# Kernel optimization log

Hardware: AMD Instinct MI355X
Metric: run time of the kernel (lower is better)

## Reference

```python
import jax, jax.numpy as jnp
import numpy as np

B, L, D = 8, 512, 128
SCALE = float(np.sqrt(D))


def setup_inputs() -> dict:
    key = jax.random.key(0)
    ks = jax.random.split(key, 12)
    s = 1.0 / np.sqrt(D)
    inp = {
        "query": jax.random.normal(ks[0], (B, L, D), jnp.float32),
        "key": jax.random.normal(ks[1], (B, L, D), jnp.float32),
        "value": jax.random.normal(ks[2], (B, L, D), jnp.float32),
        # nn.Linear weights stored torch-style as (out, in); y = x @ W.T + b
        "Wq": jax.random.uniform(ks[3], (D, D), jnp.float32, -s, s),
        "bq": jax.random.uniform(ks[4], (D,), jnp.float32, -s, s),
        "Wk": jax.random.uniform(ks[5], (D, D), jnp.float32, -s, s),
        "bk": jax.random.uniform(ks[6], (D,), jnp.float32, -s, s),
        "Wv": jax.random.uniform(ks[7], (D, D), jnp.float32, -s, s),
        "bv": jax.random.uniform(ks[8], (D,), jnp.float32, -s, s),
        "w_delta": jax.random.uniform(ks[9], (D,), jnp.float32, -s, s),
        "b_delta": jnp.zeros((), jnp.float32),
        "w_sigma": jax.random.uniform(ks[10], (D,), jnp.float32, -s, s),
        "b_sigma": jnp.zeros((), jnp.float32),
        "w_theta": jax.random.uniform(ks[11], (D,), jnp.float32, -s, s),
        "b_theta": jnp.zeros((), jnp.float32),
    }
    return inp


def reference(query, key, value, Wq, bq, Wk, bk, Wv, bv,
              w_delta, b_delta, w_sigma, b_sigma, w_theta, b_theta):
    Q = query @ Wq.T + bq          # [B,Lq,D]
    K = key @ Wk.T + bk            # [B,Lk,D]
    V = value @ Wv.T + bv          # [B,Lk,D]
    e = jnp.tanh(Q[:, :, None, :] + K[:, None, :, :])  # [B,Lq,Lk,D]
    # base (sum/scale) + three linear score heads fuse into one reduction over D
    w_all = 1.0 / SCALE + w_delta + w_sigma + w_theta   # [D]
    b_all = b_delta + b_sigma + b_theta
    combined = jnp.einsum('bqkd,d->bqk', e, w_all) + b_all
    attn = jax.nn.softmax(combined, axis=-1)            # dropout in eval mode: identity
    out = jnp.einsum('bqk,bkd->bqd', attn, V)
    return out
```

## Files before the change

### kernel.cpp

```cpp
#include <hip/hip_runtime.h>


#define BB 8
#define LL 512
#define DD 128
#define NROW (BB*LL)
#define MATN (NROW*DD)
#define KSPLIT 8

static constexpr float C1 = 2.8853900817779268f;
static constexpr float LOG2E = 1.4426950408889634f;
static constexpr float INV_SCALE = 0.08838834764831845f;

typedef float v2f __attribute__((ext_vector_type(2)));

__device__ __forceinline__ float fast_exp2(float x) { return __builtin_amdgcn_exp2f(x); }
__device__ __forceinline__ float fast_rcp(float x)  { return __builtin_amdgcn_rcpf(x); }

__device__ __forceinline__ v2f mk2(float a, float b) { v2f r; r.x = a; r.y = b; return r; }

__device__ __forceinline__ v2f fma2(v2f a, v2f b, v2f c) {
#if __has_builtin(__builtin_elementwise_fma)
    return __builtin_elementwise_fma(a, b, c);
#else
    v2f r; r.x = fmaf(a.x, b.x, c.x); r.y = fmaf(a.y, b.y, c.y); return r;
#endif
}

__global__ __launch_bounds__(256) void proj_kernel(
    const float* __restrict__ query, const float* __restrict__ key,
    const float* __restrict__ value,
    const float* __restrict__ Wq, const float* __restrict__ bq,
    const float* __restrict__ Wk, const float* __restrict__ bk,
    const float* __restrict__ Wv, const float* __restrict__ bv,
    const float* __restrict__ wd, const float* __restrict__ wsg,
    const float* __restrict__ wtt, float* __restrict__ ws)
{
    __shared__ __align__(16) float Wl[128 * 66];
    __shared__ __align__(16) float Xl[32 * 66];

    const int bx = blockIdx.x;
    const int m  = bx >> 7;
    const int r0 = (bx & 127) * 32;
    const float* X    = (m == 0) ? query : (m == 1) ? key : value;
    const float* W    = (m == 0) ? Wq    : (m == 1) ? Wk  : Wv;
    const float* bias = (m == 0) ? bq    : (m == 1) ? bk  : bv;
    const int t = threadIdx.x;

    if (bx == 0 && t < 128) {
        ws[(size_t)3 * MATN + t] =
            -2.0f * LOG2E * (INV_SCALE + wd[t] + wsg[t] + wtt[t]);
    }

    const int cg = t & 31;
    const int rg = t >> 5;

    v2f acc[4][4];
    #pragma unroll
    for (int j = 0; j < 4; ++j) {
        float bj = bias[cg + 32 * j];
        #pragma unroll
        for (int i = 0; i < 4; ++i) acc[i][j] = mk2(bj, 0.f);
    }

    const float4* Wsrc = (const float4*)W;
    const float4* Xsrc = (const float4*)X;

    for (int h = 0; h < 2; ++h) {
        __syncthreads();
        #pragma unroll
        for (int j = 0; j < 8; ++j) {
            int g = t + j * 256;
            int c = g >> 4, f4 = g & 15;
            float4 v = Wsrc[c * 32 + h * 16 + f4];
            float* dst = &Wl[c * 66 + f4 * 4];
            *(float2*)dst       = make_float2(v.x, v.y);
            *(float2*)(dst + 2) = make_float2(v.z, v.w);
        }
        #pragma unroll
        for (int j = 0; j < 2; ++j) {
            int g = t + j * 256;
            int r = g >> 4, f4 = g & 15;
            float4 v = Xsrc[(r0 + r) * 32 + h * 16 + f4];
            float* dst = &Xl[r * 66 + f4 * 4];
            *(float2*)dst       = make_float2(v.x, v.y);
            *(float2*)(dst + 2) = make_float2(v.z, v.w);
        }
        __syncthreads();

        #pragma unroll 4
        for (int dg = 0; dg < 32; ++dg) {
            v2f bf[4];
            #pragma unroll
            for (int j = 0; j < 4; ++j)
                bf[j] = *(const v2f*)&Wl[(cg + 32 * j) * 66 + 2 * dg];
            v2f af[4];
            #pragma unroll
            for (int i = 0; i < 4; ++i)
                af[i] = *(const v2f*)&Xl[(rg * 4 + i) * 66 + 2 * dg];
            #pragma unroll
            for (int i = 0; i < 4; ++i)
                #pragma unroll
                for (int j = 0; j < 4; ++j)
                    acc[i][j] = fma2(af[i], bf[j], acc[i][j]);
        }
    }

    if (m == 2) {
        float* oV = ws + (size_t)2 * MATN;
        #pragma unroll
        for (int i = 0; i < 4; ++i) {
            int r = r0 + rg * 4 + i;
            #pragma unroll
            for (int j = 0; j < 4; ++j)
                oV[(size_t)r * DD + cg + 32 * j] = acc[i][j].x + acc[i][j].y;
        }
    } else {
        float* oE = ws + (size_t)m * MATN;
        #pragma unroll
        for (int i = 0; i < 4; ++i) {
            int r = r0 + rg * 4 + i;
            #pragma unroll
            for (int j = 0; j < 4; ++j)
                oE[(size_t)r * DD + cg + 32 * j] =
                    fast_exp2(C1 * (acc[i][j].x + acc[i][j].y));
        }
    }
}

template <bool ATOMIC>
__global__ __launch_bounds__(512, 6) void attn_kernel(
    const float* __restrict__ ws, float* __restrict__ outp,
    float* __restrict__ psump)
{
    __shared__ __align__(16) float Ekt[64 * 132];
    __shared__ __align__(16) float wl[128];
    __shared__ __align__(16) float EqL[8 * 512];

    const float* Eq  = ws;
    const float* Ek  = ws + (size_t)MATN;
    const float* Vp  = ws + (size_t)2 * MATN;

    const int bx   = blockIdx.x;
    const int qblk = bx >> 3;
    const int kx   = bx & 7;
    const int b    = qblk >> 4;
    const int wave = __builtin_amdgcn_readfirstlane((int)threadIdx.x >> 6);
    const int lane = threadIdx.x & 63;
    const int qa   = qblk * 32 + wave * 4;
    const int eqo  = wave * 512;

    {
        const float4* EqW = (const float4*)(Eq + (size_t)qa * DD);
        float4 ea = EqW[2 * lane];
        float4 eb = EqW[2 * lane + 1];
        *(float4*)&EqL[eqo + 8 * lane]     = ea;
        *(float4*)&EqL[eqo + 8 * lane + 4] = eb;
    }

    {
        const float4* sK = (const float4*)(Ek + (size_t)b * (LL * DD)
                                              + (size_t)kx * 64 * DD);
        #pragma unroll
        for (int r = 0; r < 4; ++r) {
            int g = (int)threadIdx.x + r * 512;
            int row = g >> 5, c4 = g & 31;
            *(float4*)&Ekt[row * 132 + c4 * 4] = sK[g];
        }
        if (threadIdx.x < 32)
            ((float4*)wl)[threadIdx.x] =
                ((const float4*)(ws + (size_t)3 * MATN))[threadIdx.x];
    }
    __syncthreads();

    const float* krow = &Ekt[lane * 132];
    const float4* wl4 = (const float4*)wl;
    const float* eqp  = &EqL[eqo];
    float s0 = 0.f, s1 = 0.f, s2 = 0.f, s3 = 0.f;

    #pragma unroll 2
    for (int ih = 0; ih < 16; ++ih) {
        float4 k0 = *(const float4*)(krow + 8 * ih);
        float4 k1 = *(const float4*)(krow + 8 * ih + 4);
        float4 w0 = wl4[2 * ih];
        float4 w1 = wl4[2 * ih + 1];
        #define QT(SS, QQ) { \
            float4 A0 = *(const float4*)(eqp + QQ * 128 + 8 * ih); \
            float4 A1 = *(const float4*)(eqp + QQ * 128 + 8 * ih + 4); \
            float e0 = fmaf(A0.x, k0.x, 1.f), e1 = fmaf(A0.y, k0.y, 1.f); \
            float e2 = fmaf(A0.z, k0.z, 1.f), e3 = fmaf(A0.w, k0.w, 1.f); \
            float d01 = e0 * e1, d23 = e2 * e3; \
            float n01 = fmaf(w0.x, e1, w0.y * e0); \
            float n23 = fmaf(w0.z, e3, w0.w * e2); \
            float num = fmaf(n01, d23, n23 * d01); \
            SS = fmaf(num, fast_rcp(d01 * d23), SS); \
            float f0 = fmaf(A1.x, k1.x, 1.f), f1 = fmaf(A1.y, k1.y, 1.f); \
            float f2 = fmaf(A1.z, k1.z, 1.f), f3 = fmaf(A1.w, k1.w, 1.f); \
            float g01 = f0 * f1, g23 = f2 * f3; \
            float m01 = fmaf(w1.x, f1, w1.y * f0); \
            float m23 = fmaf(w1.z, f3, w1.w * f2); \
            float mum = fmaf(m01, g23, m23 * g01); \
            SS = fmaf(mum, fast_rcp(g01 * g23), SS); }
        QT(s0, 0) QT(s1, 1) QT(s2, 2) QT(s3, 3)
        #undef QT
    }
    float p0 = fast_exp2(s0);
    float p1 = fast_exp2(s1);
    float p2 = fast_exp2(s2);
    float p3 = fast_exp2(s3);

    float t0 = p0, t1 = p1, t2 = p2, t3 = p3;
    #pragma unroll
    for (int off = 32; off; off >>= 1) {
        t0 += __shfl_xor(t0, off);
        t1 += __shfl_xor(t1, off);
        t2 += __shfl_xor(t2, off);
        t3 += __shfl_xor(t3, off);
    }
    if (lane == 0) {
        if (ATOMIC) {
            atomicAdd(&psump[qa + 0], t0);
            atomicAdd(&psump[qa + 1], t1);
            atomicAdd(&psump[qa + 2], t2);
            atomicAdd(&psump[qa + 3], t3);
        } else {
            float* pp = psump + (size_t)kx * NROW + qa;
            pp[0] = t0; pp[1] = t1; pp[2] = t2; pp[3] = t3;
        }
    }

    *(float4*)&EqL[eqo + 4 * lane] = make_float4(p0, p1, p2, p3);

    const float2* __restrict__ Vg =
        (const float2*)(Vp + (size_t)b * (LL * DD) + (size_t)kx * 64 * DD);
    float2 o[4];
    #pragma unroll
    for (int qq = 0; qq < 4; ++qq) o[qq] = make_float2(0.f, 0.f);

    #pragma unroll
    for (int g = 0; g < 8; ++g) {
        float2 v[8];
        #pragma unroll
        for (int e = 0; e < 8; ++e)
            v[e] = Vg[(size_t)(8 * g + e) * 64 + lane];
        #pragma unroll
        for (int e = 0; e < 8; ++e) {
            int kidx = 8 * g + e;
            float4 pw = *(const float4*)&EqL[eqo + 4 * kidx];
            o[0].x = fmaf(pw.x, v[e].x, o[0].x); o[0].y = fmaf(pw.x, v[e].y, o[0].y);
            o[1].x = fmaf(pw.y, v[e].x, o[1].x); o[1].y = fmaf(pw.y, v[e].y, o[1].y);
            o[2].x = fmaf(pw.z, v[e].x, o[2].x); o[2].y = fmaf(pw.z, v[e].y, o[2].y);
            o[3].x = fmaf(pw.w, v[e].x, o[3].x); o[3].y = fmaf(pw.w, v[e].y, o[3].y);
        }
    }

    const int d2 = 2 * lane;
    if (ATOMIC) {
        #pragma unroll
        for (int qq = 0; qq < 4; ++qq) {
            atomicAdd(&outp[(size_t)(qa + qq) * DD + d2],     o[qq].x);
            atomicAdd(&outp[(size_t)(qa + qq) * DD + d2 + 1], o[qq].y);
        }
    } else {
        float* base = outp + (size_t)kx * MATN;
        #pragma unroll
        for (int qq = 0; qq < 4; ++qq)
            *(float2*)&base[(size_t)(qa + qq) * DD + d2] = o[qq];
    }
}

__global__ __launch_bounds__(256) void reduce_kernel(
    const float* __restrict__ part, const float* __restrict__ psumP,
    float* __restrict__ out)
{
    int t = blockIdx.x * 256 + threadIdx.x;
    const float4* p4 = (const float4*)part;
    float4 acc = make_float4(0.f, 0.f, 0.f, 0.f);
    #pragma unroll
    for (int kx = 0; kx < KSPLIT; ++kx) {
        float4 v = p4[(size_t)kx * (MATN / 4) + t];
        acc.x += v.x; acc.y += v.y; acc.z += v.z; acc.w += v.w;
    }
    int q = t >> 5;
    float s = 0.f;
    #pragma unroll
    for (int kx = 0; kx < KSPLIT; ++kx) s += psumP[(size_t)kx * NROW + q];
    float inv = fast_rcp(s);
    ((float4*)out)[t] = make_float4(acc.x * inv, acc.y * inv,
                                    acc.z * inv, acc.w * inv);
}

__global__ __launch_bounds__(256) void norm_kernel(
    float* __restrict__ out, const float* __restrict__ psumG)
{
    int t = blockIdx.x * 256 + threadIdx.x;
    float2* o2 = (float2*)out;
    int q = t >> 6;
    float inv = fast_rcp(psumG[q]);
    float2 v = o2[t];
    o2[t] = make_float2(v.x * inv, v.y * inv);
}

extern "C" void kernel_launch(void* const* d_in, const int* in_sizes, int n_in,
                              void* d_out, int out_size, void* d_ws, size_t ws_size,
                              hipStream_t stream) {
    const float* query = (const float*)d_in[0];
    const float* key_  = (const float*)d_in[1];
    const float* value = (const float*)d_in[2];
    const float* Wq    = (const float*)d_in[3];
    const float* bq    = (const float*)d_in[4];
    const float* Wk    = (const float*)d_in[5];
    const float* bk    = (const float*)d_in[6];
    const float* Wv    = (const float*)d_in[7];
    const float* bv    = (const float*)d_in[8];
    const float* wd    = (const float*)d_in[9];
    const float* wsg   = (const float*)d_in[11];
    const float* wtt   = (const float*)d_in[13];
    float* ws = (float*)d_ws;
    float* out = (float*)d_out;

    const size_t off_psum = (size_t)3 * MATN + 128;
    const size_t off_part = off_psum + (size_t)KSPLIT * NROW;
    const size_t need = (off_part + (size_t)KSPLIT * MATN) * sizeof(float);

    proj_kernel<<<384, 256, 0, stream>>>(query, key_, value,
                                         Wq, bq, Wk, bk, Wv, bv,
                                         wd, wsg, wtt, ws);
    if (ws_size >= need) {
        float* psumP = ws + off_psum;
        float* part  = ws + off_part;
        attn_kernel<false><<<1024, 512, 0, stream>>>(ws, part, psumP);
        reduce_kernel<<<512, 256, 0, stream>>>(part, psumP, out);
    } else {
        float* psumG = ws + off_psum;
        hipMemsetAsync(out, 0, (size_t)out_size * sizeof(float), stream);
        hipMemsetAsync(psumG, 0, (size_t)NROW * sizeof(float), stream);
        attn_kernel<true><<<1024, 512, 0, stream>>>(ws, out, psumG);
        norm_kernel<<<1024, 256, 0, stream>>>(out, psumG);
    }
}
```

Before: 135.2 us.

## Pack attention score math into v2f ops, drop Eq LDS staging, shrink proj tiles

The attention score loop is rewritten to use packed two-wide float FMAs, with the d-dimension permuted in Eq, Ek and the weight vector so pairs line up for the packed ops. The Eq LDS buffer is removed: query exponentials are read directly from global memory (wave-uniform) and the probabilities reuse the Ekt buffer after a barrier. This frees LDS to raise the occupancy hint from 6 to 8 blocks. The projection kernel halves its row tile to launch twice as many blocks, trading reuse of the weight tile for more parallelism.

```diff
diff --git a/kernel.cpp b/kernel.cpp
--- a/kernel.cpp
+++ b/kernel.cpp
@@ -25,6 +25,11 @@
 #else
     v2f r; r.x = fmaf(a.x, b.x, c.x); r.y = fmaf(a.y, b.y, c.y); return r;
 #endif
+}
+
+__device__ __forceinline__ int dperm(int c) {
+    const int pmap[4] = {0, 2, 1, 3};
+    return (c & ~3) | pmap[c & 3];
 }
 
 __global__ __launch_bounds__(256) void proj_kernel(
@@ -37,30 +42,30 @@
     const float* __restrict__ wtt, float* __restrict__ ws)
 {
     __shared__ __align__(16) float Wl[128 * 66];
-    __shared__ __align__(16) float Xl[32 * 66];
+    __shared__ __align__(16) float Xl[16 * 66];
 
     const int bx = blockIdx.x;
-    const int m  = bx >> 7;
-    const int r0 = (bx & 127) * 32;
+    const int m  = bx >> 8;
+    const int r0 = (bx & 255) * 16;
     const float* X    = (m == 0) ? query : (m == 1) ? key : value;
     const float* W    = (m == 0) ? Wq    : (m == 1) ? Wk  : Wv;
     const float* bias = (m == 0) ? bq    : (m == 1) ? bk  : bv;
     const int t = threadIdx.x;
 
     if (bx == 0 && t < 128) {
-        ws[(size_t)3 * MATN + t] =
+        ws[(size_t)3 * MATN + dperm(t)] =
             -2.0f * LOG2E * (INV_SCALE + wd[t] + wsg[t] + wtt[t]);
     }
 
     const int cg = t & 31;
     const int rg = t >> 5;
 
-    v2f acc[4][4];
+    v2f acc[2][4];
     #pragma unroll
     for (int j = 0; j < 4; ++j) {
         float bj = bias[cg + 32 * j];
         #pragma unroll
-        for (int i = 0; i < 4; ++i) acc[i][j] = mk2(bj, 0.f);
+        for (int i = 0; i < 2; ++i) acc[i][j] = mk2(bj, 0.f);
     }
 
     const float4* Wsrc = (const float4*)W;
@@ -77,10 +82,8 @@
             *(float2*)dst       = make_float2(v.x, v.y);
             *(float2*)(dst + 2) = make_float2(v.z, v.w);
         }
-        #pragma unroll
-        for (int j = 0; j < 2; ++j) {
-            int g = t + j * 256;
-            int r = g >> 4, f4 = g & 15;
+        {
+            int r = t >> 4, f4 = t & 15;
             float4 v = Xsrc[(r0 + r) * 32 + h * 16 + f4];
             float* dst = &Xl[r * 66 + f4 * 4];
             *(float2*)dst       = make_float2(v.x, v.y);
@@ -94,12 +97,12 @@
             #pragma unroll
             for (int j = 0; j < 4; ++j)
                 bf[j] = *(const v2f*)&Wl[(cg + 32 * j) * 66 + 2 * dg];
-            v2f af[4];
-            #pragma unroll
-            for (int i = 0; i < 4; ++i)
-                af[i] = *(const v2f*)&Xl[(rg * 4 + i) * 66 + 2 * dg];
-            #pragma unroll
-            for (int i = 0; i < 4; ++i)
+            v2f af[2];
+            #pragma unroll
+            for (int i = 0; i < 2; ++i)
+                af[i] = *(const v2f*)&Xl[(rg * 2 + i) * 66 + 2 * dg];
+            #pragma unroll
+            for (int i = 0; i < 2; ++i)
                 #pragma unroll
                 for (int j = 0; j < 4; ++j)
                     acc[i][j] = fma2(af[i], bf[j], acc[i][j]);
@@ -109,33 +112,33 @@
     if (m == 2) {
         float* oV = ws + (size_t)2 * MATN;
         #pragma unroll
-        for (int i = 0; i < 4; ++i) {
-            int r = r0 + rg * 4 + i;
+        for (int i = 0; i < 2; ++i) {
+            int r = r0 + rg * 2 + i;
             #pragma unroll
             for (int j = 0; j < 4; ++j)
                 oV[(size_t)r * DD + cg + 32 * j] = acc[i][j].x + acc[i][j].y;
         }
     } else {
         float* oE = ws + (size_t)m * MATN;
-        #pragma unroll
-        for (int i = 0; i < 4; ++i) {
-            int r = r0 + rg * 4 + i;
+        const int cp = dperm(cg);
+        #pragma unroll
+        for (int i = 0; i < 2; ++i) {
+            int r = r0 + rg * 2 + i;
             #pragma unroll
             for (int j = 0; j < 4; ++j)
-                oE[(size_t)r * DD + cg + 32 * j] =
+                oE[(size_t)r * DD + cp + 32 * j] =
                     fast_exp2(C1 * (acc[i][j].x + acc[i][j].y));
         }
     }
 }
 
 template <bool ATOMIC>
-__global__ __launch_bounds__(512, 6) void attn_kernel(
+__global__ __launch_bounds__(512, 8) void attn_kernel(
     const float* __restrict__ ws, float* __restrict__ outp,
     float* __restrict__ psump)
 {
     __shared__ __align__(16) float Ekt[64 * 132];
     __shared__ __align__(16) float wl[128];
-    __shared__ __align__(16) float EqL[8 * 512];
 
     const float* Eq  = ws;
     const float* Ek  = ws + (size_t)MATN;
@@ -148,15 +151,6 @@
     const int wave = __builtin_amdgcn_readfirstlane((int)threadIdx.x >> 6);
     const int lane = threadIdx.x & 63;
     const int qa   = qblk * 32 + wave * 4;
-    const int eqo  = wave * 512;
-
-    {
-        const float4* EqW = (const float4*)(Eq + (size_t)qa * DD);
-        float4 ea = EqW[2 * lane];
-        float4 eb = EqW[2 * lane + 1];
-        *(float4*)&EqL[eqo + 8 * lane]     = ea;
-        *(float4*)&EqL[eqo + 8 * lane + 4] = eb;
-    }
 
     {
         const float4* sK = (const float4*)(Ek + (size_t)b * (LL * DD)
@@ -175,39 +169,43 @@
 
     const float* krow = &Ekt[lane * 132];
     const float4* wl4 = (const float4*)wl;
-    const float* eqp  = &EqL[eqo];
-    float s0 = 0.f, s1 = 0.f, s2 = 0.f, s3 = 0.f;
+    const float* eqq  = Eq + (size_t)qa * DD;
+    v2f S0 = mk2(0.f, 0.f), S1 = S0, S2 = S0, S3 = S0;
 
     #pragma unroll 2
     for (int ih = 0; ih < 16; ++ih) {
-        float4 k0 = *(const float4*)(krow + 8 * ih);
-        float4 k1 = *(const float4*)(krow + 8 * ih + 4);
-        float4 w0 = wl4[2 * ih];
-        float4 w1 = wl4[2 * ih + 1];
+        float4 K0 = *(const float4*)(krow + 8 * ih);
+        float4 K1 = *(const float4*)(krow + 8 * ih + 4);
+        float4 W0 = wl4[2 * ih];
+        float4 W1 = wl4[2 * ih + 1];
+        v2f k0lo = mk2(K0.x, K0.y), k0hi = mk2(K0.z, K0.w);
+        v2f k1lo = mk2(K1.x, K1.y), k1hi = mk2(K1.z, K1.w);
+        v2f w0lo = mk2(W0.x, W0.y), w0hi = mk2(W0.z, W0.w);
+        v2f w1lo = mk2(W1.x, W1.y), w1hi = mk2(W1.z, W1.w);
         #define QT(SS, QQ) { \
-            float4 A0 = *(const float4*)(eqp + QQ * 128 + 8 * ih); \
-            float4 A1 = *(const float4*)(eqp + QQ * 128 + 8 * ih + 4); \
-            float e0 = fmaf(A0.x, k0.x, 1.f), e1 = fmaf(A0.y, k0.y, 1.f); \
-            float e2 = fmaf(A0.z, k0.z, 1.f), e3 = fmaf(A0.w, k0.w, 1.f); \
-            float d01 = e0 * e1, d23 = e2 * e3; \
-            float n01 = fmaf(w0.x, e1, w0.y * e0); \
-            float n23 = fmaf(w0.z, e3, w0.w * e2); \
-            float num = fmaf(n01, d23, n23 * d01); \
-            SS = fmaf(num, fast_rcp(d01 * d23), SS); \
-            float f0 = fmaf(A1.x, k1.x, 1.f), f1 = fmaf(A1.y, k1.y, 1.f); \
-            float f2 = fmaf(A1.z, k1.z, 1.f), f3 = fmaf(A1.w, k1.w, 1.f); \
-            float g01 = f0 * f1, g23 = f2 * f3; \
-            float m01 = fmaf(w1.x, f1, w1.y * f0); \
-            float m23 = fmaf(w1.z, f3, w1.w * f2); \
-            float mum = fmaf(m01, g23, m23 * g01); \
-            SS = fmaf(mum, fast_rcp(g01 * g23), SS); }
-        QT(s0, 0) QT(s1, 1) QT(s2, 2) QT(s3, 3)
+            float4 A0 = *(const float4*)(eqq + (QQ) * 128 + 8 * ih); \
+            float4 A1 = *(const float4*)(eqq + (QQ) * 128 + 8 * ih + 4); \
+            v2f X  = fma2(mk2(A0.x, A0.y), k0lo, mk2(1.f, 1.f)); \
+            v2f Y  = fma2(mk2(A0.z, A0.w), k0hi, mk2(1.f, 1.f)); \
+            v2f D  = X * Y;                        \
+            v2f N  = fma2(w0lo, Y, w0hi * X);      \
+            v2f NU = N * mk2(D.y, D.x); \
+            float rr = fast_rcp(D.x * D.y); \
+            SS = fma2(NU, mk2(rr, rr), SS); \
+            v2f X1  = fma2(mk2(A1.x, A1.y), k1lo, mk2(1.f, 1.f)); \
+            v2f Y1  = fma2(mk2(A1.z, A1.w), k1hi, mk2(1.f, 1.f)); \
+            v2f D1  = X1 * Y1; \
+            v2f N1  = fma2(w1lo, Y1, w1hi * X1); \
+            v2f NU1 = N1 * mk2(D1.y, D1.x); \
+            float rr1 = fast_rcp(D1.x * D1.y); \
+            SS = fma2(NU1, mk2(rr1, rr1), SS); }
+        QT(S0, 0) QT(S1, 1) QT(S2, 2) QT(S3, 3)
         #undef QT
     }
-    float p0 = fast_exp2(s0);
-    float p1 = fast_exp2(s1);
-    float p2 = fast_exp2(s2);
-    float p3 = fast_exp2(s3);
+    float p0 = fast_exp2(S0.x + S0.y);
+    float p1 = fast_exp2(S1.x + S1.y);
+    float p2 = fast_exp2(S2.x + S2.y);
+    float p3 = fast_exp2(S3.x + S3.y);
 
     float t0 = p0, t1 = p1, t2 = p2, t3 = p3;
     #pragma unroll
@@ -229,7 +227,8 @@
         }
     }
 
-    *(float4*)&EqL[eqo + 4 * lane] = make_float4(p0, p1, p2, p3);
+    __syncthreads();
+    *(float4*)&Ekt[wave * 256 + 4 * lane] = make_float4(p0, p1, p2, p3);
 
     const float2* __restrict__ Vg =
         (const float2*)(Vp + (size_t)b * (LL * DD) + (size_t)kx * 64 * DD);
@@ -246,7 +245,7 @@
         #pragma unroll
         for (int e = 0; e < 8; ++e) {
             int kidx = 8 * g + e;
-            float4 pw = *(const float4*)&EqL[eqo + 4 * kidx];
+            float4 pw = *(const float4*)&Ekt[wave * 256 + 4 * kidx];
             o[0].x = fmaf(pw.x, v[e].x, o[0].x); o[0].y = fmaf(pw.x, v[e].y, o[0].y);
             o[1].x = fmaf(pw.y, v[e].x, o[1].x); o[1].y = fmaf(pw.y, v[e].y, o[1].y);
             o[2].x = fmaf(pw.z, v[e].x, o[2].x); o[2].y = fmaf(pw.z, v[e].y, o[2].y);
@@ -323,7 +322,7 @@
     const size_t off_part = off_psum + (size_t)KSPLIT * NROW;
     const size_t need = (off_part + (size_t)KSPLIT * MATN) * sizeof(float);
 
-    proj_kernel<<<384, 256, 0, stream>>>(query, key_, value,
+    proj_kernel<<<768, 256, 0, stream>>>(query, key_, value,
                                          Wq, bq, Wk, bk, Wv, bv,
                                          wd, wsg, wtt, ws);
     if (ws_size >= need) {
```

New measurement: 173.9 us. 28.6% more time.
